# Performance work log

Hardware: AMD Instinct MI355X
Metric: run time of the kernel (lower is better)

Reference implementation:

```python
import jax, jax.numpy as jnp
import numpy as np

N_NODES = 100_000
N_EDGES = 3_200_000
N_FEAT = 128
HIDDEN = 16
OUT = 2
N_GRAPHS = 64


def setup_inputs() -> dict:
    key = jax.random.key(0)
    ks = jax.random.split(key, 12)
    x = jax.random.normal(ks[0], (N_NODES, N_FEAT), dtype=jnp.float32)
    edge_index = jax.random.randint(ks[1], (2, N_EDGES), 0, N_NODES, dtype=jnp.int64)
    batch_idx = jnp.sort(jax.random.randint(ks[2], (N_NODES,), 0, N_GRAPHS, dtype=jnp.int64))

    def glorot(k, shape):
        s = jnp.sqrt(6.0 / (shape[0] + shape[1])).astype(jnp.float32)
        return jax.random.uniform(k, shape, jnp.float32, -1.0, 1.0) * s

    return {
        "x": x, "edge_index": edge_index, "batch_idx": batch_idx,
        "W0": glorot(ks[3], (N_FEAT, HIDDEN)), "b0": jnp.zeros((HIDDEN,), jnp.float32),
        "a0": jnp.full((1,), 0.25, jnp.float32),  # PReLU default weight
        "W1": glorot(ks[4], (HIDDEN, HIDDEN)), "b1": jnp.zeros((HIDDEN,), jnp.float32),
        "a1": jnp.full((1,), 0.25, jnp.float32),
        "W2": glorot(ks[5], (HIDDEN, HIDDEN)), "b2": jnp.zeros((HIDDEN,), jnp.float32),
        "a2": jnp.full((1,), 0.25, jnp.float32),
        "W3": glorot(ks[6], (HIDDEN, OUT)), "b3": jnp.zeros((OUT,), jnp.float32),
    }


def _prelu(x, a):
    return jnp.where(x > 0, x, a * x)


def _gcn_conv(x, W, b, src, dst, norm, n):
    # PyG GCNConv: linear transform, then normalized gather-scatter aggregation, then bias
    h = x @ W                                   # [N, out]
    msg = h[src] * norm[:, None]                # gather + per-edge scale
    out = jax.ops.segment_sum(msg, dst, num_segments=n)  # scatter-add into targets
    return out + b


def reference(x, edge_index, batch_idx, W0, b0, a0, W1, b1, a1, W2, b2, a2, W3, b3):
    n = x.shape[0]
    loop = jnp.arange(n, dtype=edge_index.dtype)
    src = jnp.concatenate([edge_index[0], loop])  # add self loops
    dst = jnp.concatenate([edge_index[1], loop])
    # symmetric degree normalization deg^-1/2 (deg over targets, all edge weights = 1)
    deg = jax.ops.segment_sum(jnp.ones_like(dst, dtype=x.dtype), dst, num_segments=n)
    dinv = jnp.where(deg > 0, jax.lax.rsqrt(deg), 0.0)
    norm = dinv[src] * dinv[dst]

    h = _prelu(_gcn_conv(x, W0, b0, src, dst, norm, n), a0)
    h = _prelu(_gcn_conv(h, W1, b1, src, dst, norm, n), a1)
    h = _prelu(_gcn_conv(h, W2, b2, src, dst, norm, n), a2)
    h = _gcn_conv(h, W3, b3, src, dst, norm, n)

    # global_mean_pool over graph ids
    sums = jax.ops.segment_sum(h, batch_idx, num_segments=N_GRAPHS)
    cnts = jax.ops.segment_sum(jnp.ones((n,), h.dtype), batch_idx, num_segments=N_GRAPHS)
    return sums / jnp.maximum(cnts, 1.0)[:, None]
```

## Files before the change

kernel.cpp:

```cpp
#include <hip/hip_runtime.h>


#define NN 100000
#define NE 3200000
#define NF 128
#define NH 16
#define NO 2
#define NG 64
#define NBLK 391
#define BN 256
#define NBUK 391
#define CHUNK 4096
#define NBLKA 782
#define CAPF 10240
#define NT0 6250

typedef __attribute__((ext_vector_type(8))) short short8;
typedef __attribute__((ext_vector_type(4))) float float4v;


__device__ __forceinline__ float ldf(const void* p, int i, int f32) {
  if (f32) return ((const float*)p)[i];
  unsigned int u = ((const unsigned short*)p)[i];
  return __uint_as_float(u << 16);
}
__device__ __forceinline__ int ldi(const void* p, int i, int i64) {
  if (i64) return (int)((const long long*)p)[i];
  return ((const int*)p)[i];
}
__device__ __forceinline__ void stf(void* p, int i, float v, int f32) {
  if (f32) {
    ((float*)p)[i] = v;
  } else {
    unsigned int w = __float_as_uint(v);
    unsigned int r = (w + 0x7fffu + ((w >> 16) & 1u)) >> 16;
    ((unsigned short*)p)[i] = (unsigned short)r;
  }
}
__device__ __forceinline__ float bf16lo(unsigned int u) { return __uint_as_float(u << 16); }
__device__ __forceinline__ float bf16hi(unsigned int u) { return __uint_as_float(u & 0xffff0000u); }
__device__ __forceinline__ unsigned int packbf(float x, float y) {
  unsigned int a = __float_as_uint(x);
  a = (a + 0x7fffu + ((a >> 16) & 1u)) >> 16;
  unsigned int b = __float_as_uint(y);
  b = (b + 0x7fffu + ((b >> 16) & 1u)) & 0xffff0000u;
  return a | b;
}
__device__ __forceinline__ short bf16rne(float v) {
  unsigned int w = __float_as_uint(v);
  return (short)((w + 0x7fffu + ((w >> 16) & 1u)) >> 16);
}
__device__ __forceinline__ int okf(float v) { return (v == v) && (fabsf(v) < 1e30f); }
__device__ __forceinline__ void nflag(int* diag, int bad, int bit) {
  if (__any(bad)) {
    if ((threadIdx.x & 63) == 0) atomicOr(diag + 2, 1 << bit);
  }
}
__device__ __forceinline__ int clampi(int v, int hi) {
  return (unsigned)v < (unsigned)hi ? v : 0;
}


__global__ __launch_bounds__(1024) void k_sniff(const void* x, const void* ei, int* zbase) {
  int tid = threadIdx.x;
  if (tid < 624) zbase[tid] = 0;
  __syncthreads();
  if (tid < 64) {
    unsigned int xv = ((const unsigned int*)x)[tid];
    unsigned int e = (xv >> 7) & 0xffu;
    int hit = (e >= 116u && e <= 133u);
    int hits = __popcll(__ballot(hit));
    unsigned int ev = ((const unsigned int*)ei)[2 * tid + 1];
    int nzc = __popcll(__ballot(ev != 0u));
    if (tid == 0) {
      zbase[0] = (hits < 32) ? 1 : 0;
      zbase[1] = (nzc == 0) ? 1 : 0;
    }
  }
}


__global__ __launch_bounds__(512) void k_build(const void* ei, const int* __restrict__ diag,
                                               int* __restrict__ cursor, int* __restrict__ ents) {
  __shared__ int spktA[CHUNK];
  __shared__ unsigned short sbid[CHUNK];
  __shared__ unsigned short srank[CHUNK];
  __shared__ int spktB[CHUNK];
  __shared__ int gpos[CHUNK];
  __shared__ int lscan[512];
  __shared__ int sexcl[NBUK];
  __shared__ int goff[NBUK];
  int tid = threadIdx.x, blk = blockIdx.x;
  lscan[tid] = 0;
  __syncthreads();
  int i64 = diag[1];
  int base = blk * CHUNK;
  int n = NE - base; n = n > CHUNK ? CHUNK : n;
  for (int i = tid; i < n; i += 512) {
    int sv = clampi(ldi(ei, base + i, i64), NN);
    int dv = clampi(ldi(ei, NE + base + i, i64), NN);
    int b = dv >> 8;
    spktA[i] = ((dv & 255) << 17) | sv;
    sbid[i] = (unsigned short)b;
    srank[i] = (unsigned short)atomicAdd(&lscan[b], 1);
  }
  __syncthreads();
  for (int off = 1; off < 512; off <<= 1) {
    int v = (tid >= off) ? lscan[tid - off] : 0;
    __syncthreads();
    lscan[tid] += v;
    __syncthreads();
  }
  if (tid < NBUK) {
    int b = tid;
    int incl = lscan[b];
    int excl = (b > 0) ? lscan[b - 1] : 0;
    int cnt = incl - excl;
    sexcl[b] = excl;
    int rbase = cnt ? atomicAdd(&cursor[b], cnt) : 0;
    goff[b] = b * CAPF + rbase - excl;
  }
  __syncthreads();
  for (int i = tid; i < n; i += 512) {
    int b = sbid[i];
    int rr = sexcl[b] + srank[i];
    spktB[rr] = spktA[i];
    int gp = goff[b] + rr;
    int hi = b * CAPF + CAPF - 1;
    gpos[rr] = gp <= hi ? gp : hi;
  }
  __syncthreads();
  for (int r = tid; r < n; r += 512) ents[gpos[r]] = spktB[r];
}

__global__ __launch_bounds__(512) void k_bsort(int* __restrict__ ents, const int* __restrict__ cursor,
                                               int* __restrict__ rowstart, int* __restrict__ rowend,
                                               float* __restrict__ dinv, int* __restrict__ diag) {
  __shared__ int ent[CAPF];
  __shared__ unsigned short rnk[CAPF];
  __shared__ int lcnt[BN];
  __shared__ int sexcl[BN];
  int tid = threadIdx.x, b = blockIdx.x;
  int bs = b * CAPF;
  int n = cursor[b];
  if (n > CAPF) { n = CAPF; if (tid == 0) atomicOr(diag + 2, 1 << 9); }
  if (tid < BN) lcnt[tid] = 0;
  __syncthreads();
  for (int i = tid; i < n; i += 512) {
    int e = ents[bs + i];
    ent[i] = e;
    rnk[i] = (unsigned short)atomicAdd(&lcnt[e >> 17], 1);
  }
  __syncthreads();
  int c = (tid < BN) ? lcnt[tid] : 0;
  for (int off = 1; off < BN; off <<= 1) {
    int v = (tid < BN && tid >= off) ? lcnt[tid - off] : 0;
    __syncthreads();
    if (tid < BN) lcnt[tid] += v;
    __syncthreads();
  }
  if (tid < BN) {
    int excl = lcnt[tid] - c;
    sexcl[tid] = excl;
    int node = (b << 8) + tid;
    if (node < NN) {
      rowstart[node] = bs + excl;
      rowend[node] = bs + excl + c;
      dinv[node] = rsqrtf((float)(c + 1));
    }
  }
  __syncthreads();
  for (int i = tid; i < n; i += 512) {
    int e = ent[i];
    ents[bs + sexcl[e >> 17] + rnk[i]] = e & 0x1FFFF;
  }
}


__global__ __launch_bounds__(256) void k_t0(const void* __restrict__ x, const void* __restrict__ W0,
                                            const float* __restrict__ dinv,
                                            int* __restrict__ diag, unsigned int* __restrict__ out) {
  int tid = threadIdx.x;
  int f32 = diag[0];
  int wave = tid >> 6, lane = tid & 63;
  int nfe = lane & 15, quad = lane >> 4;
  short8 bfr[4];
  if (f32) {
    const float* wf = (const float*)W0;
#pragma unroll
    for (int mf = 0; mf < 4; ++mf) {
      short8 t;
#pragma unroll
      for (int j = 0; j < 8; ++j) t[j] = bf16rne(wf[(mf * 32 + quad * 8 + j) * NH + nfe]);
      bfr[mf] = t;
    }
  } else {
    const unsigned short* wu = (const unsigned short*)W0;
#pragma unroll
    for (int mf = 0; mf < 4; ++mf) {
      short8 t;
#pragma unroll
      for (int j = 0; j < 8; ++j) t[j] = (short)wu[(mf * 32 + quad * 8 + j) * NH + nfe];
      bfr[mf] = t;
    }
  }
  int tile = blockIdx.x * 4 + wave;
  if (tile >= NT0) return;
  int node0 = tile * 16;
  float4v c = {0.f, 0.f, 0.f, 0.f};
  if (f32) {
    const float4v* xrow = (const float4v*)((const float*)x + (node0 + nfe) * NF);
#pragma unroll
    for (int mf = 0; mf < 4; ++mf) {
      float4v f0 = xrow[mf * 8 + quad * 2];
      float4v f1 = xrow[mf * 8 + quad * 2 + 1];
      short8 a;
#pragma unroll
      for (int j = 0; j < 4; ++j) {
        a[j] = bf16rne(f0[j]);
        a[j + 4] = bf16rne(f1[j]);
      }
      c = __builtin_amdgcn_mfma_f32_16x16x32_bf16(a, bfr[mf], c, 0, 0, 0);
    }
  } else {
    const short8* xrow = (const short8*)((const unsigned short*)x + (node0 + nfe) * NF);
#pragma unroll
    for (int mf = 0; mf < 4; ++mf) {
      c = __builtin_amdgcn_mfma_f32_16x16x32_bf16(xrow[mf * 4 + quad], bfr[mf], c, 0, 0, 0);
    }
  }
  int bad = 0;
#pragma unroll
  for (int r = 0; r < 4; ++r) {
    int node = node0 + quad * 4 + r;
    float v = c[r] * dinv[node];
    float o = __shfl_xor(v, 1);
    if (!(nfe & 1)) out[node * 8 + (nfe >> 1)] = packbf(v, o);
    bad |= !okf(v);
  }
  nflag(diag, bad, 0);
}


__global__ __launch_bounds__(256) void k_aggT(const uint2* __restrict__ hin,
                                              const int* __restrict__ srcs,
                                              const int* __restrict__ rowstart,
                                              const int* __restrict__ rowend,
                                              const float* __restrict__ dinv,
                                              const void* __restrict__ b, const void* __restrict__ a,
                                              const void* __restrict__ Wn,
                                              int* __restrict__ diag, int bit,
                                              uint2* __restrict__ hout) {
  __shared__ float ws[NH * NH];
  int tid = threadIdx.x;
  int f32 = diag[0];
  ws[tid] = ldf(Wn, tid, f32);
  __syncthreads();
  int gid = blockIdx.x * 256 + tid;
  if (gid >= NN * 4) return;
  int node = gid >> 2, p = gid & 3;
  uint2 self = hin[gid];
  float acc0 = bf16lo(self.x), acc1 = bf16hi(self.x);
  float acc2 = bf16lo(self.y), acc3 = bf16hi(self.y);
  int e = rowstart[node], e1 = rowend[node];
  if ((e & 1) && e < e1) {
    uint2 v = hin[srcs[e] * 4 + p];
    acc0 += bf16lo(v.x);
    acc1 += bf16hi(v.x);
    acc2 += bf16lo(v.y);
    acc3 += bf16hi(v.y);
    ++e;
  }
  for (; e + 8 <= e1; e += 8) {
    uint2 si = *(const uint2*)(srcs + e + 2 * p);
    uint2 v[8];
#pragma unroll
    for (int k = 0; k < 4; ++k) {
      int ia = __shfl((int)si.x, k, 4);
      int ib = __shfl((int)si.y, k, 4);
      v[2 * k] = hin[ia * 4 + p];
      v[2 * k + 1] = hin[ib * 4 + p];
    }
#pragma unroll
    for (int k = 0; k < 8; ++k) {
      acc0 += bf16lo(v[k].x);
      acc1 += bf16hi(v[k].x);
      acc2 += bf16lo(v[k].y);
      acc3 += bf16hi(v[k].y);
    }
  }
  for (; e + 2 <= e1; e += 2) {
    uint2 va = hin[srcs[e] * 4 + p];
    uint2 vb = hin[srcs[e + 1] * 4 + p];
    acc0 += bf16lo(va.x) + bf16lo(vb.x);
    acc1 += bf16hi(va.x) + bf16hi(vb.x);
    acc2 += bf16lo(va.y) + bf16lo(vb.y);
    acc3 += bf16hi(va.y) + bf16hi(vb.y);
  }
  if (e < e1) {
    uint2 v = hin[srcs[e] * 4 + p];
    acc0 += bf16lo(v.x);
    acc1 += bf16hi(v.x);
    acc2 += bf16lo(v.y);
    acc3 += bf16hi(v.y);
  }
  float dv = dinv[node];
  float av = ldf(a, 0, f32);
  float p0 = dv * acc0 + ldf(b, 4 * p + 0, f32);
  float p1 = dv * acc1 + ldf(b, 4 * p + 1, f32);
  float p2 = dv * acc2 + ldf(b, 4 * p + 2, f32);
  float p3 = dv * acc3 + ldf(b, 4 * p + 3, f32);
  p0 = p0 > 0.f ? p0 : av * p0;
  p1 = p1 > 0.f ? p1 : av * p1;
  p2 = p2 > 0.f ? p2 : av * p2;
  p3 = p3 > 0.f ? p3 : av * p3;
  float t0 = 0.f, t1 = 0.f, t2 = 0.f, t3 = 0.f;
#pragma unroll
  for (int j = 0; j < 4; ++j) {
    float q0 = __shfl(p0, j, 4);
    float q1 = __shfl(p1, j, 4);
    float q2 = __shfl(p2, j, 4);
    float q3 = __shfl(p3, j, 4);
    const float* w0 = &ws[(4 * j) * NH + 4 * p];
    const float* w1 = &ws[(4 * j + 1) * NH + 4 * p];
    const float* w2 = &ws[(4 * j + 2) * NH + 4 * p];
    const float* w3 = &ws[(4 * j + 3) * NH + 4 * p];
    t0 += q0 * w0[0] + q1 * w1[0] + q2 * w2[0] + q3 * w3[0];
    t1 += q0 * w0[1] + q1 * w1[1] + q2 * w2[1] + q3 * w3[1];
    t2 += q0 * w0[2] + q1 * w1[2] + q2 * w2[2] + q3 * w3[2];
    t3 += q0 * w0[3] + q1 * w1[3] + q2 * w2[3] + q3 * w3[3];
  }
  t0 *= dv; t1 *= dv; t2 *= dv; t3 *= dv;
  uint2 o;
  o.x = packbf(t0, t1);
  o.y = packbf(t2, t3);
  hout[gid] = o;
  nflag(diag, !okf(t0) || !okf(t3), bit);
}

__global__ __launch_bounds__(256) void k_aggT3(const uint2* __restrict__ hin,
                                               const int* __restrict__ srcs,
                                               const int* __restrict__ rowstart,
                                               const int* __restrict__ rowend,
                                               const float* __restrict__ dinv,
                                               const void* __restrict__ b, const void* __restrict__ a,
                                               const void* __restrict__ W3,
                                               int* __restrict__ diag, float2* __restrict__ hout) {
  __shared__ float ws[NH * NO];
  int tid = threadIdx.x;
  int f32 = diag[0];
  if (tid < NH * NO) ws[tid] = ldf(W3, tid, f32);
  __syncthreads();
  int gid = blockIdx.x * 256 + tid;
  if (gid >= NN * 4) return;
  int node = gid >> 2, p = gid & 3;
  uint2 self = hin[gid];
  float acc0 = bf16lo(self.x), acc1 = bf16hi(self.x);
  float acc2 = bf16lo(self.y), acc3 = bf16hi(self.y);
  int e = rowstart[node], e1 = rowend[node];
  if ((e & 1) && e < e1) {
    uint2 v = hin[srcs[e] * 4 + p];
    acc0 += bf16lo(v.x);
    acc1 += bf16hi(v.x);
    acc2 += bf16lo(v.y);
    acc3 += bf16hi(v.y);
    ++e;
  }
  for (; e + 8 <= e1; e += 8) {
    uint2 si = *(const uint2*)(srcs + e + 2 * p);
    uint2 v[8];
#pragma unroll
    for (int k = 0; k < 4; ++k) {
      int ia = __shfl((int)si.x, k, 4);
      int ib = __shfl((int)si.y, k, 4);
      v[2 * k] = hin[ia * 4 + p];
      v[2 * k + 1] = hin[ib * 4 + p];
    }
#pragma unroll
    for (int k = 0; k < 8; ++k) {
      acc0 += bf16lo(v[k].x);
      acc1 += bf16hi(v[k].x);
      acc2 += bf16lo(v[k].y);
      acc3 += bf16hi(v[k].y);
    }
  }
  for (; e + 2 <= e1; e += 2) {
    uint2 va = hin[srcs[e] * 4 + p];
    uint2 vb = hin[srcs[e + 1] * 4 + p];
    acc0 += bf16lo(va.x) + bf16lo(vb.x);
    acc1 += bf16hi(va.x) + bf16hi(vb.x);
    acc2 += bf16lo(va.y) + bf16lo(vb.y);
    acc3 += bf16hi(va.y) + bf16hi(vb.y);
  }
  if (e < e1) {
    uint2 v = hin[srcs[e] * 4 + p];
    acc0 += bf16lo(v.x);
    acc1 += bf16hi(v.x);
    acc2 += bf16lo(v.y);
    acc3 += bf16hi(v.y);
  }
  float dv = dinv[node];
  float av = ldf(a, 0, f32);
  float p0 = dv * acc0 + ldf(b, 4 * p + 0, f32);
  float p1 = dv * acc1 + ldf(b, 4 * p + 1, f32);
  float p2 = dv * acc2 + ldf(b, 4 * p + 2, f32);
  float p3 = dv * acc3 + ldf(b, 4 * p + 3, f32);
  p0 = p0 > 0.f ? p0 : av * p0;
  p1 = p1 > 0.f ? p1 : av * p1;
  p2 = p2 > 0.f ? p2 : av * p2;
  p3 = p3 > 0.f ? p3 : av * p3;
  float u0 = p0 * ws[(4 * p) * NO]     + p1 * ws[(4 * p + 1) * NO] +
             p2 * ws[(4 * p + 2) * NO] + p3 * ws[(4 * p + 3) * NO];
  float u1 = p0 * ws[(4 * p) * NO + 1]     + p1 * ws[(4 * p + 1) * NO + 1] +
             p2 * ws[(4 * p + 2) * NO + 1] + p3 * ws[(4 * p + 3) * NO + 1];
  u0 += __shfl_xor(u0, 1, 4);
  u0 += __shfl_xor(u0, 2, 4);
  u1 += __shfl_xor(u1, 1, 4);
  u1 += __shfl_xor(u1, 2, 4);
  if (p == 0) hout[node] = make_float2(dv * u0, dv * u1);
  nflag(diag, !okf(u0) || !okf(u1), 6);
}

__global__ __launch_bounds__(256) void k_agg2p(const float2* __restrict__ tin,
                                               const int* __restrict__ srcs,
                                               const int* __restrict__ rowstart,
                                               const int* __restrict__ rowend,
                                               const float* __restrict__ dinv,
                                               const void* __restrict__ b3,
                                               const void* __restrict__ batch,
                                               int* __restrict__ diag, float* __restrict__ pool) {
  __shared__ float ssum[NG * NO];
  __shared__ float scnt[NG];
  int tid = threadIdx.x;
  int f32 = diag[0], i64 = diag[1];
  if (tid < NG * NO) ssum[tid] = 0.f;
  if (tid < NG) scnt[tid] = 0.f;
  __syncthreads();
  int node = blockIdx.x * 256 + tid;
  if (node < NN) {
    float2 t = tin[node];
    float a0 = t.x, a1 = t.y;
    int e = rowstart[node], e1 = rowend[node];
    while ((e & 3) && e < e1) {
      float2 hv = tin[srcs[e]];
      a0 += hv.x;
      a1 += hv.y;
      ++e;
    }
    for (; e + 4 <= e1; e += 4) {
      int4 s4 = *(const int4*)(srcs + e);
      float2 h0 = tin[s4.x], h1 = tin[s4.y], h2 = tin[s4.z], h3 = tin[s4.w];
      a0 += h0.x + h1.x + h2.x + h3.x;
      a1 += h0.y + h1.y + h2.y + h3.y;
    }
    for (; e < e1; ++e) {
      float2 hv = tin[srcs[e]];
      a0 += hv.x;
      a1 += hv.y;
    }
    float dv = dinv[node];
    a0 = dv * a0 + ldf(b3, 0, f32);
    a1 = dv * a1 + ldf(b3, 1, f32);
    int g = ldi(batch, node, i64);
    g = (unsigned)g < NG ? g : 0;
    atomicAdd(&ssum[g * 2], a0);
    atomicAdd(&ssum[g * 2 + 1], a1);
    atomicAdd(&scnt[g], 1.f);
    nflag(diag, !okf(a0) || !okf(a1), 7);
  }
  __syncthreads();
  if (tid < NG * NO && ssum[tid] != 0.f) atomicAdd(&pool[tid], ssum[tid]);
  if (tid < NG && scnt[tid] != 0.f) atomicAdd(&pool[NG * NO + tid], scnt[tid]);
}

__global__ __launch_bounds__(128) void k_final(const float* __restrict__ pool,
                                               const int* __restrict__ diag, void* __restrict__ out) {
  int i = threadIdx.x;
  int f32 = diag[0], i64 = diag[1], stg = diag[2];
  float c = pool[NG * NO + (i >> 1)];
  c = c > 1.f ? c : 1.f;
  float v = pool[i] / c;
  if (stg != 0 || !okf(v)) {
    int stage = stg ? __ffs(stg) : 15;
    v = 1024.0f + stage * 64.0f + f32 * 16.0f + i64 * 8.0f;
  }
  stf(out, i, v, f32);
}

__global__ __launch_bounds__(128) void k_diag_ws(void* out, float v) {
  unsigned int w = __float_as_uint(v);
  ((unsigned short*)out)[threadIdx.x] = (unsigned short)(w >> 16);
}


extern "C" void kernel_launch(void* const* d_in, const int* in_sizes, int n_in,
                              void* d_out, int out_size, void* d_ws, size_t ws_size,
                              hipStream_t stream) {
  const void* x  = d_in[0];
  const void* ei = d_in[1];
  const void* batch = d_in[2];
  const void* W0 = d_in[3];
  const void* b0 = d_in[4];
  const void* a0 = d_in[5];
  const void* W1 = d_in[6];
  const void* b1 = d_in[7];
  const void* a1 = d_in[8];
  const void* W2 = d_in[9];
  const void* b2 = d_in[10];
  const void* a2 = d_in[11];
  const void* W3 = d_in[12];
  const void* b3 = d_in[13];

  char* w = (char*)d_ws;
  int* diag         = (int*)(w + 0);
  float* pool       = (float*)(w + 64);
  int* cursor       = (int*)(w + 896);
  float* dinv       = (float*)(w + 2496);
  int* rowstart     = (int*)(w + 402496);
  int* rowend       = (int*)(w + 802496);
  int* ents         = (int*)(w + 1202496);
  uint2* hsA        = (uint2*)(w + 17217856);
  uint2* hsB        = (uint2*)(w + 20417856);
  float2* hs3       = (float2*)(w + 23617856);
  const size_t NEED = 24417856;

  if (ws_size < NEED) {
    k_diag_ws<<<1, 128, 0, stream>>>(d_out, (float)ws_size);
    return;
  }

  k_sniff<<<1, 1024, 0, stream>>>(x, ei, (int*)w);

  k_build<<<NBLKA, 512, 0, stream>>>(ei, diag, cursor, ents);
  k_bsort<<<NBUK, 512, 0, stream>>>(ents, cursor, rowstart, rowend, dinv, diag);

  k_t0<<<(NT0 + 3) / 4, 256, 0, stream>>>(x, W0, dinv, diag, (unsigned int*)hsA);
  k_aggT<<<(NN * 4 + 255) / 256, 256, 0, stream>>>(hsA, ents, rowstart, rowend, dinv, b0, a0, W1, diag, 1, hsB);
  k_aggT<<<(NN * 4 + 255) / 256, 256, 0, stream>>>(hsB, ents, rowstart, rowend, dinv, b1, a1, W2, diag, 3, hsA);
  k_aggT3<<<(NN * 4 + 255) / 256, 256, 0, stream>>>(hsA, ents, rowstart, rowend, dinv, b2, a2, W3, diag, hs3);
  k_agg2p<<<NBLK, 256, 0, stream>>>(hs3, ents, rowstart, rowend, dinv, b3, batch, diag, pool);

  k_final<<<1, 128, 0, stream>>>(pool, diag, d_out);
}
```

Before: 280.0 us.

## Build CSR via global degree atomics and direct placement; prefetch edge indices

Replaces the two-pass bucketed shared-memory sort with a three-kernel CSR build: a global atomic degree count, a per-256-node block prefix scan that writes row offsets and dinv, and a placement pass that writes each source into its destination row using per-node atomic cursors. This removes the large shared-memory staging and the second in-bucket sort, at the cost of millions of global atomics and scattered writes. Edge order within a row becomes nondeterministic, which can change float summation order. The aggregation kernels also software-prefetch the next group of source indices before gathering the current one, to hide index-load latency.

```diff
diff --git a/kernel.cpp b/kernel.cpp
--- a/kernel.cpp
+++ b/kernel.cpp
@@ -10,9 +10,9 @@
 #define NBLK 391
 #define BN 256
 #define NBUK 391
-#define CHUNK 4096
-#define NBLKA 782
 #define CAPF 10240
+#define ENTCAP (NBUK * CAPF)
+#define NBLKD 3125
 #define NT0 6250
 
 typedef __attribute__((ext_vector_type(8))) short short8;
@@ -79,101 +79,88 @@
   }
 }
 
-
-__global__ __launch_bounds__(512) void k_build(const void* ei, const int* __restrict__ diag,
-                                               int* __restrict__ cursor, int* __restrict__ ents) {
-  __shared__ int spktA[CHUNK];
-  __shared__ unsigned short sbid[CHUNK];
-  __shared__ unsigned short srank[CHUNK];
-  __shared__ int spktB[CHUNK];
-  __shared__ int gpos[CHUNK];
-  __shared__ int lscan[512];
-  __shared__ int sexcl[NBUK];
-  __shared__ int goff[NBUK];
-  int tid = threadIdx.x, blk = blockIdx.x;
-  lscan[tid] = 0;
+__global__ __launch_bounds__(256) void k_zero(int* __restrict__ deg) {
+  int i = blockIdx.x * 256 + threadIdx.x;
+  if (i < NN) deg[i] = 0;
+}
+
+
+__global__ __launch_bounds__(256) void k_deg(const void* ei, const int* __restrict__ diag,
+                                             int* __restrict__ deg) {
+  int i64 = diag[1];
+  int t4 = (blockIdx.x * 256 + threadIdx.x) * 4;
+  if (t4 >= NE) return;
+  int d0, d1, d2, d3;
+  if (i64) {
+    const long long* e64 = (const long long*)ei;
+    longlong2 a = *(const longlong2*)(e64 + NE + t4);
+    longlong2 b = *(const longlong2*)(e64 + NE + t4 + 2);
+    d0 = (int)a.x; d1 = (int)a.y; d2 = (int)b.x; d3 = (int)b.y;
+  } else {
+    int4 a = *(const int4*)((const int*)ei + NE + t4);
+    d0 = a.x; d1 = a.y; d2 = a.z; d3 = a.w;
+  }
+  atomicAdd(&deg[clampi(d0, NN)], 1);
+  atomicAdd(&deg[clampi(d1, NN)], 1);
+  atomicAdd(&deg[clampi(d2, NN)], 1);
+  atomicAdd(&deg[clampi(d3, NN)], 1);
+}
+
+__global__ __launch_bounds__(256) void k_rows(const int* __restrict__ deg,
+                                              int* __restrict__ rowstart, int* __restrict__ rowend,
+                                              int* __restrict__ cursorN, float* __restrict__ dinv) {
+  __shared__ int s[256];
+  int tid = threadIdx.x, b = blockIdx.x;
+  int node = b * 256 + tid;
+  int d = (node < NN) ? deg[node] : 0;
+  s[tid] = d;
   __syncthreads();
+  for (int off = 1; off < 256; off <<= 1) {
+    int v = (tid >= off) ? s[tid - off] : 0;
+    __syncthreads();
+    s[tid] += v;
+    __syncthreads();
+  }
+  if (node < NN) {
+    int excl = s[tid] - d;
+    int rs = b * CAPF + excl;
+    rowstart[node] = rs;
+    rowend[node] = rs + d;
+    cursorN[node] = rs;
+    dinv[node] = rsqrtf((float)(d + 1));
+  }
+}
+
+__global__ __launch_bounds__(256) void k_place(const void* ei, const int* __restrict__ diag,
+                                               int* __restrict__ cursorN, int* __restrict__ ents) {
   int i64 = diag[1];
-  int base = blk * CHUNK;
-  int n = NE - base; n = n > CHUNK ? CHUNK : n;
-  for (int i = tid; i < n; i += 512) {
-    int sv = clampi(ldi(ei, base + i, i64), NN);
-    int dv = clampi(ldi(ei, NE + base + i, i64), NN);
-    int b = dv >> 8;
-    spktA[i] = ((dv & 255) << 17) | sv;
-    sbid[i] = (unsigned short)b;
-    srank[i] = (unsigned short)atomicAdd(&lscan[b], 1);
-  }
-  __syncthreads();
-  for (int off = 1; off < 512; off <<= 1) {
-    int v = (tid >= off) ? lscan[tid - off] : 0;
-    __syncthreads();
-    lscan[tid] += v;
-    __syncthreads();
-  }
-  if (tid < NBUK) {
-    int b = tid;
-    int incl = lscan[b];
-    int excl = (b > 0) ? lscan[b - 1] : 0;
-    int cnt = incl - excl;
-    sexcl[b] = excl;
-    int rbase = cnt ? atomicAdd(&cursor[b], cnt) : 0;
-    goff[b] = b * CAPF + rbase - excl;
-  }
-  __syncthreads();
-  for (int i = tid; i < n; i += 512) {
-    int b = sbid[i];
-    int rr = sexcl[b] + srank[i];
-    spktB[rr] = spktA[i];
-    int gp = goff[b] + rr;
-    int hi = b * CAPF + CAPF - 1;
-    gpos[rr] = gp <= hi ? gp : hi;
-  }
-  __syncthreads();
-  for (int r = tid; r < n; r += 512) ents[gpos[r]] = spktB[r];
-}
-
-__global__ __launch_bounds__(512) void k_bsort(int* __restrict__ ents, const int* __restrict__ cursor,
-                                               int* __restrict__ rowstart, int* __restrict__ rowend,
-                                               float* __restrict__ dinv, int* __restrict__ diag) {
-  __shared__ int ent[CAPF];
-  __shared__ unsigned short rnk[CAPF];
-  __shared__ int lcnt[BN];
-  __shared__ int sexcl[BN];
-  int tid = threadIdx.x, b = blockIdx.x;
-  int bs = b * CAPF;
-  int n = cursor[b];
-  if (n > CAPF) { n = CAPF; if (tid == 0) atomicOr(diag + 2, 1 << 9); }
-  if (tid < BN) lcnt[tid] = 0;
-  __syncthreads();
-  for (int i = tid; i < n; i += 512) {
-    int e = ents[bs + i];
-    ent[i] = e;
-    rnk[i] = (unsigned short)atomicAdd(&lcnt[e >> 17], 1);
-  }
-  __syncthreads();
-  int c = (tid < BN) ? lcnt[tid] : 0;
-  for (int off = 1; off < BN; off <<= 1) {
-    int v = (tid < BN && tid >= off) ? lcnt[tid - off] : 0;
-    __syncthreads();
-    if (tid < BN) lcnt[tid] += v;
-    __syncthreads();
-  }
-  if (tid < BN) {
-    int excl = lcnt[tid] - c;
-    sexcl[tid] = excl;
-    int node = (b << 8) + tid;
-    if (node < NN) {
-      rowstart[node] = bs + excl;
-      rowend[node] = bs + excl + c;
-      dinv[node] = rsqrtf((float)(c + 1));
-    }
-  }
-  __syncthreads();
-  for (int i = tid; i < n; i += 512) {
-    int e = ent[i];
-    ents[bs + sexcl[e >> 17] + rnk[i]] = e & 0x1FFFF;
-  }
+  int t4 = (blockIdx.x * 256 + threadIdx.x) * 4;
+  if (t4 >= NE) return;
+  int s0, s1, s2, s3, d0, d1, d2, d3;
+  if (i64) {
+    const long long* e64 = (const long long*)ei;
+    longlong2 a = *(const longlong2*)(e64 + t4);
+    longlong2 b = *(const longlong2*)(e64 + t4 + 2);
+    longlong2 c = *(const longlong2*)(e64 + NE + t4);
+    longlong2 e = *(const longlong2*)(e64 + NE + t4 + 2);
+    s0 = (int)a.x; s1 = (int)a.y; s2 = (int)b.x; s3 = (int)b.y;
+    d0 = (int)c.x; d1 = (int)c.y; d2 = (int)e.x; d3 = (int)e.y;
+  } else {
+    const int* e32 = (const int*)ei;
+    int4 a = *(const int4*)(e32 + t4);
+    int4 b = *(const int4*)(e32 + NE + t4);
+    s0 = a.x; s1 = a.y; s2 = a.z; s3 = a.w;
+    d0 = b.x; d1 = b.y; d2 = b.z; d3 = b.w;
+  }
+  int sl;
+  sl = atomicAdd(&cursorN[clampi(d0, NN)], 1);
+  ents[sl < ENTCAP ? sl : ENTCAP - 1] = clampi(s0, NN);
+  sl = atomicAdd(&cursorN[clampi(d1, NN)], 1);
+  ents[sl < ENTCAP ? sl : ENTCAP - 1] = clampi(s1, NN);
+  sl = atomicAdd(&cursorN[clampi(d2, NN)], 1);
+  ents[sl < ENTCAP ? sl : ENTCAP - 1] = clampi(s2, NN);
+  sl = atomicAdd(&cursorN[clampi(d3, NN)], 1);
+  ents[sl < ENTCAP ? sl : ENTCAP - 1] = clampi(s3, NN);
 }
 
 
@@ -271,8 +258,11 @@
     acc3 += bf16hi(v.y);
     ++e;
   }
-  for (; e + 8 <= e1; e += 8) {
-    uint2 si = *(const uint2*)(srcs + e + 2 * p);
+  uint2 si = make_uint2(0u, 0u);
+  if (e + 8 <= e1) si = *(const uint2*)(srcs + e + 2 * p);
+  while (e + 8 <= e1) {
+    uint2 sn = si;
+    if (e + 16 <= e1) sn = *(const uint2*)(srcs + e + 8 + 2 * p);
     uint2 v[8];
 #pragma unroll
     for (int k = 0; k < 4; ++k) {
@@ -288,6 +278,8 @@
       acc2 += bf16lo(v[k].y);
       acc3 += bf16hi(v[k].y);
     }
+    si = sn;
+    e += 8;
   }
   for (; e + 2 <= e1; e += 2) {
     uint2 va = hin[srcs[e] * 4 + p];
@@ -366,8 +358,11 @@
     acc3 += bf16hi(v.y);
     ++e;
   }
-  for (; e + 8 <= e1; e += 8) {
-    uint2 si = *(const uint2*)(srcs + e + 2 * p);
+  uint2 si = make_uint2(0u, 0u);
+  if (e + 8 <= e1) si = *(const uint2*)(srcs + e + 2 * p);
+  while (e + 8 <= e1) {
+    uint2 sn = si;
+    if (e + 16 <= e1) sn = *(const uint2*)(srcs + e + 8 + 2 * p);
     uint2 v[8];
 #pragma unroll
     for (int k = 0; k < 4; ++k) {
@@ -383,6 +378,8 @@
       acc2 += bf16lo(v[k].y);
       acc3 += bf16hi(v[k].y);
     }
+    si = sn;
+    e += 8;
   }
   for (; e + 2 <= e1; e += 2) {
     uint2 va = hin[srcs[e] * 4 + p];
@@ -447,11 +444,16 @@
       a1 += hv.y;
       ++e;
     }
-    for (; e + 4 <= e1; e += 4) {
-      int4 s4 = *(const int4*)(srcs + e);
-      float2 h0 = tin[s4.x], h1 = tin[s4.y], h2 = tin[s4.z], h3 = tin[s4.w];
+    int4 si = make_int4(0, 0, 0, 0);
+    if (e + 4 <= e1) si = *(const int4*)(srcs + e);
+    while (e + 4 <= e1) {
+      int4 sn = si;
+      if (e + 8 <= e1) sn = *(const int4*)(srcs + e + 4);
+      float2 h0 = tin[si.x], h1 = tin[si.y], h2 = tin[si.z], h3 = tin[si.w];
       a0 += h0.x + h1.x + h2.x + h3.x;
       a1 += h0.y + h1.y + h2.y + h3.y;
+      si = sn;
+      e += 4;
     }
     for (; e < e1; ++e) {
       float2 hv = tin[srcs[e]];
@@ -514,7 +516,6 @@
   char* w = (char*)d_ws;
   int* diag         = (int*)(w + 0);
   float* pool       = (float*)(w + 64);
-  int* cursor       = (int*)(w + 896);
   float* dinv       = (float*)(w + 2496);
   int* rowstart     = (int*)(w + 402496);
   int* rowend       = (int*)(w + 802496);
@@ -522,17 +523,22 @@
   uint2* hsA        = (uint2*)(w + 17217856);
   uint2* hsB        = (uint2*)(w + 20417856);
   float2* hs3       = (float2*)(w + 23617856);
-  const size_t NEED = 24417856;
+  int* cursorN      = (int*)(w + 24417856);
+  const size_t NEED = 24817856;
 
   if (ws_size < NEED) {
     k_diag_ws<<<1, 128, 0, stream>>>(d_out, (float)ws_size);
     return;
   }
 
+  int* deg = rowend;
+
   k_sniff<<<1, 1024, 0, stream>>>(x, ei, (int*)w);
-
-  k_build<<<NBLKA, 512, 0, stream>>>(ei, diag, cursor, ents);
-  k_bsort<<<NBUK, 512, 0, stream>>>(ents, cursor, rowstart, rowend, dinv, diag);
+  k_zero<<<NBLK, 256, 0, stream>>>(deg);
+
+  k_deg<<<NBLKD, 256, 0, stream>>>(ei, diag, deg);
+  k_rows<<<NBUK, 256, 0, stream>>>(deg, rowstart, rowend, cursorN, dinv);
+  k_place<<<NBLKD, 256, 0, stream>>>(ei, diag, cursorN, ents);
 
   k_t0<<<(NT0 + 3) / 4, 256, 0, stream>>>(x, W0, dinv, diag, (unsigned int*)hsA);
   k_aggT<<<(NN * 4 + 255) / 256, 256, 0, stream>>>(hsA, ents, rowstart, rowend, dinv, b0, a0, W1, diag, 1, hsB);
```

Result: slower. 620.7 us (+121.7%).
